# Performance work log

Hardware: AMD Instinct MI355X
Metric: run time of the kernel (lower is better)

Reference implementation:

```python
import jax, jax.numpy as jnp
import numpy as np

B, L, H = 1024, 256, 128
NUM_TEAMS, NUM_VENUES, NUM_RESULTS = 1000, 3, 3
OUT_IN = 4 * H + 2 + 3  # past_repr (4H+2) concat stats (3)


def setup_inputs() -> dict:
    key = jax.random.key(0)
    ks = jax.random.split(key, 16)
    return {
        "team_embed": jax.random.normal(ks[0], (NUM_TEAMS, H), jnp.float32) * 0.02,
        "venue_embed": jax.random.normal(ks[1], (NUM_VENUES, H), jnp.float32) * 0.02,
        "result_embed": jax.random.normal(ks[2], (NUM_RESULTS, H), jnp.float32) * 0.02,
        "W_out": jax.random.normal(ks[3], (OUT_IN, NUM_RESULTS), jnp.float32) * 0.02,
        "b_out": jnp.zeros((NUM_RESULTS,), jnp.float32),
        "goals_for": jax.random.uniform(ks[4], (B, L), jnp.float32) * 5.0,
        "goals_against": jax.random.uniform(ks[5], (B, L), jnp.float32) * 5.0,
        "stats": jax.random.uniform(ks[6], (B, 3), jnp.float32),
        "venue": jax.random.randint(ks[7], (B, L), 0, NUM_VENUES),
        "team": jax.random.randint(ks[8], (B, L), 0, NUM_TEAMS),
        "opponent": jax.random.randint(ks[9], (B, L), 0, NUM_TEAMS),
        "result": jax.random.randint(ks[10], (B, L), 0, NUM_RESULTS),
        "next_venue": jax.random.randint(ks[11], (B,), 0, NUM_VENUES),
        "next_team": jax.random.randint(ks[12], (B,), 0, NUM_TEAMS),
        "next_opponent": jax.random.randint(ks[13], (B,), 0, NUM_TEAMS),
    }


def reference(team_embed, venue_embed, result_embed, W_out, b_out,
              goals_for, goals_against, stats,
              venue, team, opponent, result,
              next_venue, next_team, next_opponent):
    h = team_embed.shape[1]
    # (B, L, 4H+2): embedding gathers + goal scalars concatenated
    past_seq = jnp.concatenate([
        venue_embed[venue], team_embed[team], team_embed[opponent],
        result_embed[result], goals_for[..., None], goals_against[..., None],
    ], axis=-1)
    # (B, 3H): next-match condition vector
    next_cond = jnp.concatenate([
        venue_embed[next_venue], team_embed[next_team], team_embed[next_opponent],
    ], axis=-1)
    scale = jnp.asarray(3 * h, past_seq.dtype) ** 0.5
    scores = jnp.einsum('bld,bd->bl', past_seq[..., : 3 * h], next_cond) / scale
    attn = jax.nn.softmax(scores, axis=1)                 # over L
    past_repr = jnp.einsum('bl,bld->bd', attn, past_seq)  # (B, 4H+2)
    logits = jnp.concatenate([past_repr, stats], axis=-1) @ W_out + b_out
    return logits
```

## Files before the change

### kernel.cpp

```cpp
#include <hip/hip_runtime.h>

#define L_ 256
#define H_ 128

#define KSCALE 0.07362222315f

__global__ __launch_bounds__(256) void fused_match_kernel(
    const float* __restrict__ team_embed,
    const float* __restrict__ venue_embed,
    const float* __restrict__ result_embed,
    const float* __restrict__ W_out,
    const float* __restrict__ b_out,
    const float* __restrict__ goals_for,
    const float* __restrict__ goals_against,
    const float* __restrict__ stats,
    const int* __restrict__ venue,
    const int* __restrict__ team,
    const int* __restrict__ opponent,
    const int* __restrict__ result,
    const int* __restrict__ next_venue,
    const int* __restrict__ next_team,
    const int* __restrict__ next_opponent,
    float* __restrict__ out)
{
    const int b    = blockIdx.x;
    const int t    = threadIdx.x;
    const int lane = t & 63;
    const int wid  = t >> 6;
    const int half = lane >> 5;
    const int c    = lane & 31;

    __shared__ float  nc[384];
    __shared__ int    s_team[L_];
    __shared__ int    s_opp[L_];
    __shared__ float  s_score[L_];
    __shared__ float  s_dv[L_];
    __shared__ float  s_dotv[3];
    __shared__ float  s_m[8];
    __shared__ float4 s_accT[8][32];
    __shared__ float4 s_accO[8][32];
    __shared__ float  s_reds[4];
    __shared__ float  s_redw[4][8];
    __shared__ float  s_w[8];
    __shared__ float  s_pr[517];

    const int base = b * L_;
    const int my_venue  = venue[base + t];
    const int my_result = result[base + t];
    const float my_gf   = goals_for[base + t];
    const float my_ga   = goals_against[base + t];
    s_team[t] = team[base + t];
    s_opp[t]  = opponent[base + t];

    const int nv  = next_venue[b];
    const int ntm = next_team[b];
    const int nop = next_opponent[b];
    if (t < 128) {
        nc[t]       = venue_embed[nv * H_ + t];
        nc[128 + t] = team_embed[ntm * H_ + t];
    } else {
        nc[128 + t] = team_embed[nop * H_ + (t - 128)];
    }
    __syncthreads();

    if (wid < 3) {
        float a = venue_embed[wid * H_ + lane]      * nc[lane]
                + venue_embed[wid * H_ + 64 + lane] * nc[64 + lane];
        #pragma unroll
        for (int off = 32; off > 0; off >>= 1) a += __shfl_down(a, off);
        if (lane == 0) s_dotv[wid] = a;
    }
    __syncthreads();
    s_dv[t] = s_dotv[my_venue];
    __syncthreads();

    const float4 nct_c = ((const float4*)(nc + 128))[c];
    const float4 nco_c = ((const float4*)(nc + 256))[c];
    const int    lb    = wid * 64 + half * 32;
    float4 accT = make_float4(0.f, 0.f, 0.f, 0.f);
    float4 accO = make_float4(0.f, 0.f, 0.f, 0.f);
    float  mrun = -1e30f;
    #pragma unroll 4
    for (int i = 0; i < 32; ++i) {
        const int l = lb + i;
        const float4 vT = ((const float4*)team_embed)[s_team[l] * 32 + c];
        const float4 vO = ((const float4*)team_embed)[s_opp[l]  * 32 + c];
        float p = vT.x * nct_c.x + vT.y * nct_c.y + vT.z * nct_c.z + vT.w * nct_c.w
                + vO.x * nco_c.x + vO.y * nco_c.y + vO.z * nco_c.z + vO.w * nco_c.w;
        #pragma unroll
        for (int k = 16; k > 0; k >>= 1) p += __shfl_xor(p, k);
        const float kk = (p + s_dv[l]) * KSCALE;
        if ((lane & 31) == 0) s_score[l] = kk;
        if (kk > mrun) {
            const float alpha = exp2f(mrun - kk);
            accT.x *= alpha; accT.y *= alpha; accT.z *= alpha; accT.w *= alpha;
            accO.x *= alpha; accO.y *= alpha; accO.z *= alpha; accO.w *= alpha;
            mrun = kk;
        }
        const float e = exp2f(kk - mrun);
        accT.x += e * vT.x; accT.y += e * vT.y; accT.z += e * vT.z; accT.w += e * vT.w;
        accO.x += e * vO.x; accO.y += e * vO.y; accO.z += e * vO.z; accO.w += e * vO.w;
    }
    {
        const int hw = wid * 2 + half;
        if ((lane & 31) == 0) s_m[hw] = mrun;
        s_accT[hw][c] = accT;
        s_accO[hw][c] = accO;
    }
    __syncthreads();

    float M = s_m[0];
    #pragma unroll
    for (int j = 1; j < 8; ++j) M = fmaxf(M, s_m[j]);

    const float e = exp2f(s_score[t] - M);
    float vals[8];
    vals[0] = (my_venue  == 0) ? e : 0.f;
    vals[1] = (my_venue  == 1) ? e : 0.f;
    vals[2] = (my_venue  == 2) ? e : 0.f;
    vals[3] = (my_result == 0) ? e : 0.f;
    vals[4] = (my_result == 1) ? e : 0.f;
    vals[5] = (my_result == 2) ? e : 0.f;
    vals[6] = e * my_gf;
    vals[7] = e * my_ga;
    float sum = e;
    #pragma unroll
    for (int off = 32; off > 0; off >>= 1) {
        sum += __shfl_down(sum, off);
        #pragma unroll
        for (int k = 0; k < 8; ++k) vals[k] += __shfl_down(vals[k], off);
    }
    if (lane == 0) {
        s_reds[wid] = sum;
        #pragma unroll
        for (int k = 0; k < 8; ++k) s_redw[wid][k] = vals[k];
    }
    __syncthreads();
    const float Z    = s_reds[0] + s_reds[1] + s_reds[2] + s_reds[3];
    const float invZ = 1.f / Z;
    if (t < 8)
        s_w[t] = (s_redw[0][t] + s_redw[1][t] + s_redw[2][t] + s_redw[3][t]) * invZ;
    __syncthreads();

    if (t < 64) {
        const int seg = t >> 5;
        const int cc  = t & 31;
        float4 a = make_float4(0.f, 0.f, 0.f, 0.f);
        #pragma unroll
        for (int h = 0; h < 8; ++h) {
            const float sc  = exp2f(s_m[h] - M);
            const float4 v  = seg ? s_accO[h][cc] : s_accT[h][cc];
            a.x += sc * v.x; a.y += sc * v.y; a.z += sc * v.z; a.w += sc * v.w;
        }
        const int d = 128 + seg * 128 + cc * 4;
        s_pr[d + 0] = a.x * invZ;
        s_pr[d + 1] = a.y * invZ;
        s_pr[d + 2] = a.z * invZ;
        s_pr[d + 3] = a.w * invZ;
        if (t < 2) s_pr[512 + t] = s_w[6 + t];
        if (t >= 2 && t < 5) s_pr[512 + t] = stats[b * 3 + t - 2];
    } else if (t < 192) {
        const int j = t - 64;
        s_pr[j] = s_w[0] * venue_embed[j] + s_w[1] * venue_embed[H_ + j]
                + s_w[2] * venue_embed[2 * H_ + j];
    } else {
        const int j = t - 192;
        s_pr[384 + j] = s_w[3] * result_embed[j]      + s_w[4] * result_embed[H_ + j]
                      + s_w[5] * result_embed[2 * H_ + j];
        s_pr[448 + j] = s_w[3] * result_embed[64 + j] + s_w[4] * result_embed[H_ + 64 + j]
                      + s_w[5] * result_embed[2 * H_ + 64 + j];
    }
    __syncthreads();

    if (wid < 3) {
        float acc = 0.f;
        for (int d = lane; d < 517; d += 64) acc += s_pr[d] * W_out[d * 3 + wid];
        #pragma unroll
        for (int off = 32; off > 0; off >>= 1) acc += __shfl_down(acc, off);
        if (lane == 0) out[b * 3 + wid] = acc + b_out[wid];
    }
}

extern "C" void kernel_launch(void* const* d_in, const int* in_sizes, int n_in,
                              void* d_out, int out_size, void* d_ws, size_t ws_size,
                              hipStream_t stream) {
    const float* team_embed    = (const float*)d_in[0];
    const float* venue_embed   = (const float*)d_in[1];
    const float* result_embed  = (const float*)d_in[2];
    const float* W_out         = (const float*)d_in[3];
    const float* b_out         = (const float*)d_in[4];
    const float* goals_for     = (const float*)d_in[5];
    const float* goals_against = (const float*)d_in[6];
    const float* stats         = (const float*)d_in[7];
    const int* venue           = (const int*)d_in[8];
    const int* team            = (const int*)d_in[9];
    const int* opponent        = (const int*)d_in[10];
    const int* result          = (const int*)d_in[11];
    const int* next_venue      = (const int*)d_in[12];
    const int* next_team       = (const int*)d_in[13];
    const int* next_opponent   = (const int*)d_in[14];
    float* out = (float*)d_out;

    const int B = in_sizes[12];
    fused_match_kernel<<<B, 256, 0, stream>>>(
        team_embed, venue_embed, result_embed, W_out, b_out,
        goals_for, goals_against, stats,
        venue, team, opponent, result,
        next_venue, next_team, next_opponent, out);
}
```

Before: 106.7 us.

## Use 16-lane row groups with DPP reductions instead of shuffle trees

Each wave now handles 4 sequence positions at a time with 16 lanes per row, and each lane loads two float4 chunks per embedding row. This halves the depth of the cross-lane score reduction and raises the number of outstanding gathers per lane. All shuffle-based reductions are replaced with DPP row/broadcast adds, so the reduced value lands in lane 63. In exchange the kernel uses more registers (four float4 accumulators per lane) and doubles the partial-state shared memory and the merge loop to 16 groups.

Result: faster. 101.9 us (-4.6%).

```diff
diff --git a/kernel.cpp b/kernel.cpp
--- a/kernel.cpp
+++ b/kernel.cpp
@@ -4,6 +4,27 @@
 #define H_ 128
 
 #define KSCALE 0.07362222315f
+
+template <int CTRL>
+__device__ __forceinline__ float dpp_add(float v) {
+    return v + __int_as_float(__builtin_amdgcn_update_dpp(
+        0, __float_as_int(v), CTRL, 0xF, 0xF, true));
+}
+
+__device__ __forceinline__ float dppReduce16(float v) {
+    v = dpp_add<0xB1>(v);
+    v = dpp_add<0x4E>(v);
+    v = dpp_add<0x141>(v);
+    v = dpp_add<0x140>(v);
+    return v;
+}
+
+__device__ __forceinline__ float dppReduce64(float v) {
+    v = dppReduce16(v);
+    v = dpp_add<0x142>(v);
+    v = dpp_add<0x143>(v);
+    return v;
+}
 
 __global__ __launch_bounds__(256) void fused_match_kernel(
     const float* __restrict__ team_embed,
@@ -27,8 +48,8 @@
     const int t    = threadIdx.x;
     const int lane = t & 63;
     const int wid  = t >> 6;
-    const int half = lane >> 5;
-    const int c    = lane & 31;
+    const int grp  = lane >> 4;
+    const int ci   = lane & 15;
 
     __shared__ float  nc[384];
     __shared__ int    s_team[L_];
@@ -36,9 +57,9 @@
     __shared__ float  s_score[L_];
     __shared__ float  s_dv[L_];
     __shared__ float  s_dotv[3];
-    __shared__ float  s_m[8];
-    __shared__ float4 s_accT[8][32];
-    __shared__ float4 s_accO[8][32];
+    __shared__ float  s_m[16];
+    __shared__ float4 s_accT[16][32];
+    __shared__ float4 s_accO[16][32];
     __shared__ float  s_reds[4];
     __shared__ float  s_redw[4][8];
     __shared__ float  s_w[8];
@@ -66,52 +87,67 @@
     if (wid < 3) {
         float a = venue_embed[wid * H_ + lane]      * nc[lane]
                 + venue_embed[wid * H_ + 64 + lane] * nc[64 + lane];
-        #pragma unroll
-        for (int off = 32; off > 0; off >>= 1) a += __shfl_down(a, off);
-        if (lane == 0) s_dotv[wid] = a;
+        a = dppReduce64(a);
+        if (lane == 63) s_dotv[wid] = a;
     }
     __syncthreads();
     s_dv[t] = s_dotv[my_venue];
     __syncthreads();
 
-    const float4 nct_c = ((const float4*)(nc + 128))[c];
-    const float4 nco_c = ((const float4*)(nc + 256))[c];
-    const int    lb    = wid * 64 + half * 32;
-    float4 accT = make_float4(0.f, 0.f, 0.f, 0.f);
-    float4 accO = make_float4(0.f, 0.f, 0.f, 0.f);
+    const float4 nct0 = ((const float4*)(nc + 128))[ci];
+    const float4 nct1 = ((const float4*)(nc + 128))[ci + 16];
+    const float4 nco0 = ((const float4*)(nc + 256))[ci];
+    const float4 nco1 = ((const float4*)(nc + 256))[ci + 16];
+
+    const int lb = wid * 64;
+    float4 accT0 = make_float4(0.f, 0.f, 0.f, 0.f);
+    float4 accT1 = make_float4(0.f, 0.f, 0.f, 0.f);
+    float4 accO0 = make_float4(0.f, 0.f, 0.f, 0.f);
+    float4 accO1 = make_float4(0.f, 0.f, 0.f, 0.f);
     float  mrun = -1e30f;
-    #pragma unroll 4
-    for (int i = 0; i < 32; ++i) {
-        const int l = lb + i;
-        const float4 vT = ((const float4*)team_embed)[s_team[l] * 32 + c];
-        const float4 vO = ((const float4*)team_embed)[s_opp[l]  * 32 + c];
-        float p = vT.x * nct_c.x + vT.y * nct_c.y + vT.z * nct_c.z + vT.w * nct_c.w
-                + vO.x * nco_c.x + vO.y * nco_c.y + vO.z * nco_c.z + vO.w * nco_c.w;
-        #pragma unroll
-        for (int k = 16; k > 0; k >>= 1) p += __shfl_xor(p, k);
+    #pragma unroll 2
+    for (int i = 0; i < 16; ++i) {
+        const int l = lb + i * 4 + grp;
+        const float4* rT = (const float4*)team_embed + s_team[l] * 32;
+        const float4* rO = (const float4*)team_embed + s_opp[l]  * 32;
+        const float4 vT0 = rT[ci];
+        const float4 vT1 = rT[ci + 16];
+        const float4 vO0 = rO[ci];
+        const float4 vO1 = rO[ci + 16];
+        float p = vT0.x * nct0.x + vT0.y * nct0.y + vT0.z * nct0.z + vT0.w * nct0.w
+                + vT1.x * nct1.x + vT1.y * nct1.y + vT1.z * nct1.z + vT1.w * nct1.w
+                + vO0.x * nco0.x + vO0.y * nco0.y + vO0.z * nco0.z + vO0.w * nco0.w
+                + vO1.x * nco1.x + vO1.y * nco1.y + vO1.z * nco1.z + vO1.w * nco1.w;
+        p = dppReduce16(p);
         const float kk = (p + s_dv[l]) * KSCALE;
-        if ((lane & 31) == 0) s_score[l] = kk;
+        if (ci == 0) s_score[l] = kk;
         if (kk > mrun) {
             const float alpha = exp2f(mrun - kk);
-            accT.x *= alpha; accT.y *= alpha; accT.z *= alpha; accT.w *= alpha;
-            accO.x *= alpha; accO.y *= alpha; accO.z *= alpha; accO.w *= alpha;
+            accT0.x *= alpha; accT0.y *= alpha; accT0.z *= alpha; accT0.w *= alpha;
+            accT1.x *= alpha; accT1.y *= alpha; accT1.z *= alpha; accT1.w *= alpha;
+            accO0.x *= alpha; accO0.y *= alpha; accO0.z *= alpha; accO0.w *= alpha;
+            accO1.x *= alpha; accO1.y *= alpha; accO1.z *= alpha; accO1.w *= alpha;
             mrun = kk;
         }
         const float e = exp2f(kk - mrun);
-        accT.x += e * vT.x; accT.y += e * vT.y; accT.z += e * vT.z; accT.w += e * vT.w;
-        accO.x += e * vO.x; accO.y += e * vO.y; accO.z += e * vO.z; accO.w += e * vO.w;
+        accT0.x += e * vT0.x; accT0.y += e * vT0.y; accT0.z += e * vT0.z; accT0.w += e * vT0.w;
+        accT1.x += e * vT1.x; accT1.y += e * vT1.y; accT1.z += e * vT1.z; accT1.w += e * vT1.w;
+        accO0.x += e * vO0.x; accO0.y += e * vO0.y; accO0.z += e * vO0.z; accO0.w += e * vO0.w;
+        accO1.x += e * vO1.x; accO1.y += e * vO1.y; accO1.z += e * vO1.z; accO1.w += e * vO1.w;
     }
     {
-        const int hw = wid * 2 + half;
-        if ((lane & 31) == 0) s_m[hw] = mrun;
-        s_accT[hw][c] = accT;
-        s_accO[hw][c] = accO;
+        const int hs = wid * 4 + grp;
+        if (ci == 0) s_m[hs] = mrun;
+        s_accT[hs][ci]      = accT0;
+        s_accT[hs][ci + 16] = accT1;
+        s_accO[hs][ci]      = accO0;
+        s_accO[hs][ci + 16] = accO1;
     }
     __syncthreads();
 
     float M = s_m[0];
     #pragma unroll
-    for (int j = 1; j < 8; ++j) M = fmaxf(M, s_m[j]);
+    for (int j = 1; j < 16; ++j) M = fmaxf(M, s_m[j]);
 
     const float e = exp2f(s_score[t] - M);
     float vals[8];
@@ -123,14 +159,10 @@
     vals[5] = (my_result == 2) ? e : 0.f;
     vals[6] = e * my_gf;
     vals[7] = e * my_ga;
-    float sum = e;
+    float sum = dppReduce64(e);
     #pragma unroll
-    for (int off = 32; off > 0; off >>= 1) {
-        sum += __shfl_down(sum, off);
-        #pragma unroll
-        for (int k = 0; k < 8; ++k) vals[k] += __shfl_down(vals[k], off);
-    }
-    if (lane == 0) {
+    for (int k = 0; k < 8; ++k) vals[k] = dppReduce64(vals[k]);
+    if (lane == 63) {
         s_reds[wid] = sum;
         #pragma unroll
         for (int k = 0; k < 8; ++k) s_redw[wid][k] = vals[k];
@@ -147,7 +179,7 @@
         const int cc  = t & 31;
         float4 a = make_float4(0.f, 0.f, 0.f, 0.f);
         #pragma unroll
-        for (int h = 0; h < 8; ++h) {
+        for (int h = 0; h < 16; ++h) {
             const float sc  = exp2f(s_m[h] - M);
             const float4 v  = seg ? s_accO[h][cc] : s_accT[h][cc];
             a.x += sc * v.x; a.y += sc * v.y; a.z += sc * v.z; a.w += sc * v.w;
@@ -175,9 +207,8 @@
     if (wid < 3) {
         float acc = 0.f;
         for (int d = lane; d < 517; d += 64) acc += s_pr[d] * W_out[d * 3 + wid];
-        #pragma unroll
-        for (int off = 32; off > 0; off >>= 1) acc += __shfl_down(acc, off);
-        if (lane == 0) out[b * 3 + wid] = acc + b_out[wid];
+        acc = dppReduce64(acc);
+        if (lane == 63) out[b * 3 + wid] = acc + b_out[wid];
     }
 }
 
```
